# Kernel tuning notes

Hardware: AMD Instinct MI355X
Metric: run time of the kernel (lower is better)

## Reference

```python
import jax, jax.numpy as jnp
import numpy as np

S, B, D, H, V = 1024, 4, 1024, 4096, 32000
EPS = 1e-5

def _ln(x, g, b):
    m = jnp.mean(x, axis=-1, keepdims=True)
    v = jnp.var(x, axis=-1, keepdims=True)
    return (x - m) * jax.lax.rsqrt(v + EPS) * g + b

def setup_inputs() -> dict:
    key = jax.random.key(0)
    ks = jax.random.split(key, 12)
    def xav(k, shape):
        fan_in, fan_out = shape[1], shape[0]
        lim = np.sqrt(6.0 / (fan_in + fan_out))
        return jax.random.uniform(k, shape, jnp.float32, -lim, lim)
    return {
        "inputs": jax.random.randint(ks[0], (S, B), 0, V, dtype=jnp.int32),
        "emb_table": jax.random.normal(ks[1], (V, D), jnp.float32),
        "WQ": xav(ks[2], (D, D)),
        "WK": xav(ks[3], (D, D)),
        "WV": xav(ks[4], (D, D)),
        "Wo": xav(ks[5], (D, D)),
        "bo": jnp.zeros((D,), jnp.float32),
        "W1": xav(ks[6], (H, D)),
        "b1": jnp.zeros((H,), jnp.float32),
        "W2": xav(ks[7], (D, H)),
        "b2": jnp.zeros((D,), jnp.float32),
        "g1": jnp.ones((D,), jnp.float32),
        "be1": jnp.zeros((D,), jnp.float32),
        "g2": jnp.ones((D,), jnp.float32),
        "be2": jnp.zeros((D,), jnp.float32),
        "Wd": xav(ks[8], (V, D)),
        "bd": jnp.zeros((V,), jnp.float32),
    }

def reference(inputs, emb_table, WQ, WK, WV, Wo, bo, W1, b1, W2, b2, g1, be1, g2, be2, Wd, bd):
    # inputs: [S, B] int ids
    emb = emb_table[inputs]                       # [S, B, D]
    # F.linear(x, W) == x @ W.T
    Q = jnp.einsum('sbd,ed->bse', emb, WQ)        # [B, S, D]
    K = jnp.einsum('sbd,ed->bse', emb, WK)
    Vv = jnp.einsum('sbd,ed->bse', emb, WV)
    scores = jnp.einsum('bqd,bkd->bqk', Q, K) / jnp.sqrt(jnp.float32(D))
    attn = jax.nn.softmax(scores, axis=-1)        # [B, S, S]
    z = jnp.einsum('bqk,bkd->qbd', attn, Vv)      # back to [S, B, D]
    z = jnp.einsum('sbd,ed->sbe', z, Wo) + bo
    x = _ln(emb + z, g1, be1)
    ffn = jnp.einsum('sbh,dh->sbd', jax.nn.relu(jnp.einsum('sbd,hd->sbh', x, W1) + b1), W2) + b2
    out = _ln(x + ffn, g2, be2)
    logits = out.reshape(S * B, D) @ Wd.T + bd    # [S*B, V]
    return logits
```

## Files before the change

kernel.cpp:

```cpp
#include <hip/hip_runtime.h>

typedef float f32x4 __attribute__((ext_vector_type(4)));
typedef __bf16 bf16x8 __attribute__((ext_vector_type(8)));
typedef int i32x4 __attribute__((ext_vector_type(4)));
typedef unsigned short u16;
typedef unsigned short u16x4 __attribute__((ext_vector_type(4)));
typedef unsigned short u16x8 __attribute__((ext_vector_type(8)));
typedef unsigned int u32;

#define SEQ 1024
#define NBATCH 4
#define DM 1024
#define HD 4096
#define NV 32000
#define NT (SEQ * NBATCH)

__device__ __forceinline__ u16 f2bf(float f) {
  u32 u = __builtin_bit_cast(u32, f);
  return (u16)((u + 0x7FFFu + ((u >> 16) & 1u)) >> 16);
}

__global__ __launch_bounds__(256) void cast_bf16_kernel(const float* __restrict__ in,
                                                        u16* __restrict__ out, int n8) {
  int i = blockIdx.x * 256 + threadIdx.x;
  if (i >= n8) return;
  const f32x4* p = (const f32x4*)(in + (long)i * 8);
  f32x4 a = p[0], b = p[1];
  u16x8 o;
  o[0] = f2bf(a[0]); o[1] = f2bf(a[1]); o[2] = f2bf(a[2]); o[3] = f2bf(a[3]);
  o[4] = f2bf(b[0]); o[5] = f2bf(b[1]); o[6] = f2bf(b[2]); o[7] = f2bf(b[3]);
  *(u16x8*)(out + (long)i * 8) = o;
}

__global__ __launch_bounds__(256) void embed_kernel(const int* __restrict__ ids,
                                                    const float* __restrict__ tab,
                                                    float* __restrict__ ef,
                                                    u16* __restrict__ eh) {
  int t = blockIdx.x, tid = threadIdx.x;
  long id = ids[t];
  f32x4 v = *(const f32x4*)(tab + id * DM + tid * 4);
  *(f32x4*)(ef + (long)t * DM + tid * 4) = v;
  u16x4 h;
  h[0] = f2bf(v[0]); h[1] = f2bf(v[1]); h[2] = f2bf(v[2]); h[3] = f2bf(v[3]);
  *(u16x4*)(eh + (long)t * DM + tid * 4) = h;
}

__global__ __launch_bounds__(256) void softmax_kernel(const float* __restrict__ s,
                                                      u16* __restrict__ p) {
  int row = blockIdx.x, tid = threadIdx.x;
  const float* rp = s + (long)row * SEQ;
  f32x4 v = *(const f32x4*)(rp + tid * 4);
  float mx = fmaxf(fmaxf(v[0], v[1]), fmaxf(v[2], v[3]));
  for (int o = 32; o; o >>= 1) mx = fmaxf(mx, __shfl_xor(mx, o));
  __shared__ float red[4];
  if ((tid & 63) == 0) red[tid >> 6] = mx;
  __syncthreads();
  mx = fmaxf(fmaxf(red[0], red[1]), fmaxf(red[2], red[3]));
  const float sc = 0.03125f;
  f32x4 e;
  e[0] = expf((v[0] - mx) * sc); e[1] = expf((v[1] - mx) * sc);
  e[2] = expf((v[2] - mx) * sc); e[3] = expf((v[3] - mx) * sc);
  float sm = e[0] + e[1] + e[2] + e[3];
  for (int o = 32; o; o >>= 1) sm += __shfl_xor(sm, o);
  __syncthreads();
  if ((tid & 63) == 0) red[tid >> 6] = sm;
  __syncthreads();
  sm = red[0] + red[1] + red[2] + red[3];
  float inv = 1.0f / sm;
  u16x4 o4;
  o4[0] = f2bf(e[0] * inv); o4[1] = f2bf(e[1] * inv);
  o4[2] = f2bf(e[2] * inv); o4[3] = f2bf(e[3] * inv);
  *(u16x4*)(p + (long)row * SEQ + tid * 4) = o4;
}

__global__ __launch_bounds__(256) void ln_kernel(const float* __restrict__ in,
                                                 const float* __restrict__ g,
                                                 const float* __restrict__ be,
                                                 float* __restrict__ outf,
                                                 u16* __restrict__ outh) {
  int row = blockIdx.x, tid = threadIdx.x;
  f32x4 v = *(const f32x4*)(in + (long)row * DM + tid * 4);
  float s = v[0] + v[1] + v[2] + v[3];
  float q = v[0] * v[0] + v[1] * v[1] + v[2] * v[2] + v[3] * v[3];
  for (int o = 32; o; o >>= 1) { s += __shfl_xor(s, o); q += __shfl_xor(q, o); }
  __shared__ float rs_[4], rq_[4];
  if ((tid & 63) == 0) { rs_[tid >> 6] = s; rq_[tid >> 6] = q; }
  __syncthreads();
  s = rs_[0] + rs_[1] + rs_[2] + rs_[3];
  q = rq_[0] + rq_[1] + rq_[2] + rq_[3];
  float mean = s * (1.0f / DM);
  float var = q * (1.0f / DM) - mean * mean;
  float rstd = rsqrtf(var + 1e-5f);
  f32x4 gg = *(const f32x4*)(g + tid * 4);
  f32x4 bb = *(const f32x4*)(be + tid * 4);
  f32x4 y;
  y[0] = (v[0] - mean) * rstd * gg[0] + bb[0];
  y[1] = (v[1] - mean) * rstd * gg[1] + bb[1];
  y[2] = (v[2] - mean) * rstd * gg[2] + bb[2];
  y[3] = (v[3] - mean) * rstd * gg[3] + bb[3];
  if (outf) *(f32x4*)(outf + (long)row * DM + tid * 4) = y;
  if (outh) {
    u16x4 h;
    h[0] = f2bf(y[0]); h[1] = f2bf(y[1]); h[2] = f2bf(y[2]); h[3] = f2bf(y[3]);
    *(u16x4*)(outh + (long)row * DM + tid * 4) = h;
  }
}

__global__ __launch_bounds__(256) void ln_i8_kernel(const float* __restrict__ in,
                                                    const float* __restrict__ g,
                                                    const float* __restrict__ be,
                                                    char* __restrict__ q8,
                                                    float* __restrict__ scale) {
  int row = blockIdx.x, tid = threadIdx.x;
  f32x4 v = *(const f32x4*)(in + (long)row * DM + tid * 4);
  float s = v[0] + v[1] + v[2] + v[3];
  float q = v[0] * v[0] + v[1] * v[1] + v[2] * v[2] + v[3] * v[3];
  for (int o = 32; o; o >>= 1) { s += __shfl_xor(s, o); q += __shfl_xor(q, o); }
  __shared__ float rs_[4], rq_[4], rm_[4];
  if ((tid & 63) == 0) { rs_[tid >> 6] = s; rq_[tid >> 6] = q; }
  __syncthreads();
  s = rs_[0] + rs_[1] + rs_[2] + rs_[3];
  q = rq_[0] + rq_[1] + rq_[2] + rq_[3];
  float mean = s * (1.0f / DM);
  float var = q * (1.0f / DM) - mean * mean;
  float rstd = rsqrtf(var + 1e-5f);
  f32x4 gg = *(const f32x4*)(g + tid * 4);
  f32x4 bb = *(const f32x4*)(be + tid * 4);
  f32x4 y;
  y[0] = (v[0] - mean) * rstd * gg[0] + bb[0];
  y[1] = (v[1] - mean) * rstd * gg[1] + bb[1];
  y[2] = (v[2] - mean) * rstd * gg[2] + bb[2];
  y[3] = (v[3] - mean) * rstd * gg[3] + bb[3];
  float am = fmaxf(fmaxf(fabsf(y[0]), fabsf(y[1])), fmaxf(fabsf(y[2]), fabsf(y[3])));
  for (int o = 32; o; o >>= 1) am = fmaxf(am, __shfl_xor(am, o));
  __syncthreads();
  if ((tid & 63) == 0) rm_[tid >> 6] = am;
  __syncthreads();
  am = fmaxf(fmaxf(rm_[0], rm_[1]), fmaxf(rm_[2], rm_[3]));
  float inv = (am > 0.f) ? 127.f / am : 0.f;
  int q0 = (int)rintf(y[0] * inv), q1 = (int)rintf(y[1] * inv);
  int q2 = (int)rintf(y[2] * inv), q3 = (int)rintf(y[3] * inv);
  u32 pk = (q0 & 255) | ((q1 & 255) << 8) | ((q2 & 255) << 16) | ((u32)(q3 & 255) << 24);
  *(u32*)(q8 + (size_t)row * DM + tid * 4) = pk;
  if (tid == 0) scale[row] = am * (1.0f / 127.f);
}

__global__ __launch_bounds__(256) void rowq_i8_kernel(const float* __restrict__ in,
                                                      char* __restrict__ q8,
                                                      float* __restrict__ scale) {
  int row = blockIdx.x, tid = threadIdx.x;
  f32x4 v = *(const f32x4*)(in + (size_t)row * DM + tid * 4);
  float am = fmaxf(fmaxf(fabsf(v[0]), fabsf(v[1])), fmaxf(fabsf(v[2]), fabsf(v[3])));
  for (int o = 32; o; o >>= 1) am = fmaxf(am, __shfl_xor(am, o));
  __shared__ float rm_[4];
  if ((tid & 63) == 0) rm_[tid >> 6] = am;
  __syncthreads();
  am = fmaxf(fmaxf(rm_[0], rm_[1]), fmaxf(rm_[2], rm_[3]));
  float inv = (am > 0.f) ? 127.f / am : 0.f;
  int q0 = (int)rintf(v[0] * inv), q1 = (int)rintf(v[1] * inv);
  int q2 = (int)rintf(v[2] * inv), q3 = (int)rintf(v[3] * inv);
  u32 pk = (q0 & 255) | ((q1 & 255) << 8) | ((q2 & 255) << 16) | ((u32)(q3 & 255) << 24);
  *(u32*)(q8 + (size_t)row * DM + tid * 4) = pk;
  if (tid == 0) scale[row] = am * (1.0f / 127.f);
}

#define GLD(gp, lp)                                              \
  __builtin_amdgcn_global_load_lds(                              \
      (__attribute__((address_space(1))) void*)(gp),             \
      (__attribute__((address_space(3))) void*)(lp), 16, 0, 0)

#define BM 128
#define BN 128
#define BK 32

__global__ __launch_bounds__(256) void gemm_bt(
    const u16* __restrict__ A, const u16* __restrict__ B,
    float* __restrict__ Cf, u16* __restrict__ Ch,
    const float* __restrict__ bias, const float* __restrict__ resid,
    int K, int lda, int ldb, int ldc,
    long batA, long batB, long batC, int relu) {
  __shared__ u16 As[BM * BK];
  __shared__ u16 Bs[BN * BK];
  const int tid = threadIdx.x;
  const int bz = blockIdx.z;
  A += (long)bz * batA;
  B += (long)bz * batB;
  const long cbase = (long)bz * batC;
  const int row0 = blockIdx.y * BM;
  const int col0 = blockIdx.x * BN;
  const int l = tid & 63;
  const int w = tid >> 6;
  const int wr = (w >> 1) * 64, wc = (w & 1) * 64;

  f32x4 acc[4][4] = {};

  const u16* gA = A + (long)(row0 + (tid >> 2)) * lda + (tid & 3) * 8;
  const u16* gB = B + (long)(col0 + (tid >> 2)) * ldb + (tid & 3) * 8;
  const long a64 = (long)64 * lda, b64 = (long)64 * ldb;
  u16* lA = As + tid * 8;
  u16* lB = Bs + tid * 8;

  const int fr = l & 15;
  const int fk = (l >> 4) * 8;
  const u16* rA = As + (wr + fr) * BK + fk;
  const u16* rB = Bs + (wc + fr) * BK + fk;

  for (int k0 = 0; k0 < K; k0 += BK) {
    GLD(gA + k0, lA);
    GLD(gA + a64 + k0, lA + 2048);
    GLD(gB + k0, lB);
    GLD(gB + b64 + k0, lB + 2048);
    __syncthreads();
    bf16x8 af[4], bf[4];
#pragma unroll
    for (int m = 0; m < 4; ++m) af[m] = *(const bf16x8*)(rA + m * 16 * BK);
#pragma unroll
    for (int n = 0; n < 4; ++n) bf[n] = *(const bf16x8*)(rB + n * 16 * BK);
#pragma unroll
    for (int m = 0; m < 4; ++m)
#pragma unroll
      for (int n = 0; n < 4; ++n)
        acc[m][n] = __builtin_amdgcn_mfma_f32_16x16x32_bf16(af[m], bf[n], acc[m][n], 0, 0, 0);
    __syncthreads();
  }

  const int er = row0 + wr + ((l >> 4) << 2);
  const int ec = col0 + wc + (l & 15);
#pragma unroll
  for (int m = 0; m < 4; ++m) {
#pragma unroll
    for (int n = 0; n < 4; ++n) {
      f32x4 v = acc[m][n];
      const int c = ec + n * 16;
      float bv = bias ? bias[c] : 0.0f;
#pragma unroll
      for (int i = 0; i < 4; ++i) {
        const int r = er + m * 16 + i;
        float x = v[i] + bv;
        if (resid) x += resid[(long)r * ldc + c];
        if (relu) x = fmaxf(x, 0.0f);
        if (Cf) Cf[cbase + (long)r * ldc + c] = x;
        if (Ch) Ch[cbase + (long)r * ldc + c] = f2bf(x);
      }
    }
  }
}

__global__ __launch_bounds__(256) void gemm_i8(
    const char* __restrict__ A, const char* __restrict__ B,
    float* __restrict__ C, const float* __restrict__ sA, const float* __restrict__ sB,
    const float* __restrict__ bias, int K, int lda, int ldb, int ldc,
    int Mtiles, int Ntiles) {
  __shared__ __align__(16) char As[128 * 64];
  __shared__ __align__(16) char Bs[128 * 64];
  const int tid = threadIdx.x;

  const int nwg = gridDim.x;
  const int blk = blockIdx.x;
  const int cpx = nwg >> 3;
  const int wg = (blk & 7) * cpx + (blk >> 3);
  const int gsz = 4 * Ntiles;
  const int gid = wg / gsz;
  const int rem = wg - gid * gsz;
  const int row0 = (gid * 4 + (rem & 3)) * 128;
  const int col0 = (rem >> 2) * 128;

  const int l = tid & 63;
  const int w = tid >> 6;
  const int wr = (w >> 1) * 64, wc = (w & 1) * 64;

  const int srow = tid >> 2;
  const int sslot = (tid & 3) ^ ((srow >> 1) & 3);
  const char* gA = A + (size_t)(row0 + srow) * lda + sslot * 16;
  const char* gB = B + (size_t)(col0 + srow) * ldb + sslot * 16;
  const size_t a64 = (size_t)64 * lda, b64 = (size_t)64 * ldb;
  char* lA = As + tid * 16;
  char* lB = Bs + tid * 16;

  const int fr = l & 15;
  const int fsw = 16 * ((l >> 4) ^ ((fr >> 1) & 3));
  const char* rA = As + (wr + fr) * 64 + fsw;
  const char* rB = Bs + (wc + fr) * 64 + fsw;

  i32x4 acc[4][4] = {};

  for (int k0 = 0; k0 < K; k0 += 64) {
    GLD(gA + k0, lA);
    GLD(gA + a64 + k0, lA + 4096);
    GLD(gB + k0, lB);
    GLD(gB + b64 + k0, lB + 4096);
    __syncthreads();
    i32x4 af[4], bf[4];
#pragma unroll
    for (int m = 0; m < 4; ++m) af[m] = *(const i32x4*)(rA + m * 16 * 64);
#pragma unroll
    for (int n = 0; n < 4; ++n) bf[n] = *(const i32x4*)(rB + n * 16 * 64);
#pragma unroll
    for (int m = 0; m < 4; ++m)
#pragma unroll
      for (int n = 0; n < 4; ++n)
        acc[m][n] = __builtin_amdgcn_mfma_i32_16x16x64_i8(af[m], bf[n], acc[m][n], 0, 0, 0);
    __syncthreads();
  }

  const int er = row0 + wr + ((l >> 4) << 2);
  const int ec = col0 + wc + (l & 15);
#pragma unroll
  for (int m = 0; m < 4; ++m) {
#pragma unroll
    for (int n = 0; n < 4; ++n) {
      i32x4 v = acc[m][n];
      const int c = ec + n * 16;
      const float sb = sB[c];
      const float bv = bias ? bias[c] : 0.0f;
#pragma unroll
      for (int i = 0; i < 4; ++i) {
        const int r = er + m * 16 + i;
        C[(size_t)r * ldc + c] = (float)v[i] * (sA[r] * sb) + bv;
      }
    }
  }
}

#define DSB() __builtin_amdgcn_sched_barrier(0)
#define SBAR() __builtin_amdgcn_s_barrier()

template <int N0, int N1>
__device__ __forceinline__ void mfma16(f32x4 (&acc)[8][4], const bf16x8 (&af)[8],
                                       bf16x8 b0, bf16x8 b1) {
#pragma unroll
  for (int m = 0; m < 8; ++m) {
    acc[m][N0] = __builtin_amdgcn_mfma_f32_16x16x32_bf16(af[m], b0, acc[m][N0], 0, 0, 0);
    acc[m][N1] = __builtin_amdgcn_mfma_f32_16x16x32_bf16(af[m], b1, acc[m][N1], 0, 0, 0);
  }
}

__global__ __launch_bounds__(512, 2) void gemm256_bt(
    const u16* __restrict__ A, const u16* __restrict__ B,
    float* __restrict__ Cf, u16* __restrict__ Ch,
    const float* __restrict__ bias,
    int K, int lda, int ldb, int ldc, int Mtiles, int Ntiles, int relu) {
  __shared__ __align__(16) u16 As[2][2][128 * 64];
  __shared__ __align__(16) u16 Bs[2][2][256 * 32];
  const int tid = threadIdx.x;

  const int nwg = gridDim.x;
  const int blk = blockIdx.x;
  const int cpx = nwg >> 3;
  const int wg = (blk & 7) * cpx + (blk >> 3);
  const int gsz = 4 * Ntiles;
  const int gid = wg / gsz;
  const int rem = wg - gid * gsz;
  const int row0 = (gid * 4 + (rem & 3)) * 256;
  const int col0 = (rem >> 2) * 256;

  const int l = tid & 63;
  const int w = tid >> 6;
  const int wr = w >> 2;
  const int wc = w & 3;

  const int sArow = tid >> 3;
  const int sAcol = ((tid & 7) ^ ((sArow >> 1) & 7)) * 8;
  const int sBrow = tid >> 2;
  const int sBcol = ((tid & 3) ^ ((sBrow >> 2) & 3)) * 8;

  const u16* gA = A + (size_t)(row0 + sArow) * lda + sAcol;
  const u16* gB = B + (size_t)(col0 + sBrow) * ldb + sBcol;
  const size_t a64 = (size_t)64 * lda;
  const size_t b128 = (size_t)128 * ldb;

#define STAGE_A(buf, h, kt)                                          \
  do {                                                               \
    const u16* _g = gA + (size_t)(h) * 128 * lda + (size_t)(kt) * 64;\
    u16* _l = &As[buf][h][0] + tid * 8;                              \
    GLD(_g, _l);                                                     \
    GLD(_g + a64, _l + 4096);                                        \
  } while (0)
#define STAGE_B(buf, kk, kt)                                         \
  do {                                                               \
    const u16* _g = gB + (size_t)(kt) * 64 + (kk) * 32;              \
    u16* _l = &Bs[buf][kk][0] + tid * 8;                             \
    GLD(_g, _l);                                                     \
    GLD(_g + b128, _l + 4096);                                       \
  } while (0)

  const int fr = l & 15;
  const int g8 = (l >> 4) * 8;
  const int acp0 = g8 ^ (((fr >> 1) & 7) * 8);
  const int acp1 = (32 + g8) ^ (((fr >> 1) & 7) * 8);
  const int bcp = g8 ^ (((fr >> 2) & 3) * 8);

#define RA(buf, m, cp) (*(const bf16x8*)(&As[buf][wr][((m) * 16 + fr) * 64 + (cp)]))
#define RB(buf, n, kk) (*(const bf16x8*)(&Bs[buf][kk][(wc * 64 + (n) * 16 + fr) * 32 + bcp]))

  f32x4 acc[8][4] = {};
  bf16x8 a0[8], a1[8], bb0, bb1;

  const int nkt = K >> 6;
  const int nit = nkt >> 1;

  STAGE_A(0, 0, 0); STAGE_A(0, 1, 0);
  STAGE_B(0, 0, 0); STAGE_B(0, 1, 0);
  STAGE_B(1, 0, 1); STAGE_A(1, 0, 1);
  asm volatile("s_waitcnt vmcnt(4)"); DSB();
  SBAR();

  for (int i = 0; i < nit; ++i) {
    const int u = 2 * i + 1;
    const int v = (2 * i + 2 < nkt) ? 2 * i + 2 : nkt - 1;
    const int w2 = (2 * i + 3 < nkt) ? 2 * i + 3 : nkt - 1;

#pragma unroll
    for (int m = 0; m < 8; ++m) a0[m] = RA(0, m, acp0);
    bb0 = RB(0, 0, 0); bb1 = RB(0, 1, 0);
    STAGE_A(1, 1, u);
    SBAR();
    asm volatile("s_waitcnt lgkmcnt(0)"); DSB();
    __builtin_amdgcn_s_setprio(1);
    mfma16<0, 1>(acc, a0, bb0, bb1);
    __builtin_amdgcn_s_setprio(0);
    SBAR();
    bb0 = RB(0, 2, 0); bb1 = RB(0, 3, 0);
    STAGE_B(1, 1, u);
    asm volatile("s_waitcnt vmcnt(6)"); DSB();
    SBAR();
    asm volatile("s_waitcnt lgkmcnt(0)"); DSB();
    __builtin_amdgcn_s_setprio(1);
    mfma16<2, 3>(acc, a0, bb0, bb1);
    __builtin_amdgcn_s_setprio(0);
    SBAR();
#pragma unroll
    for (int m = 0; m < 8; ++m) a1[m] = RA(0, m, acp1);
    bb0 = RB(0, 0, 1); bb1 = RB(0, 1, 1);
    STAGE_B(0, 0, v);
    SBAR();
    asm volatile("s_waitcnt lgkmcnt(0)"); DSB();
    __builtin_amdgcn_s_setprio(1);
    mfma16<0, 1>(acc, a1, bb0, bb1);
    __builtin_amdgcn_s_setprio(0);
    SBAR();
    bb0 = RB(0, 2, 1); bb1 = RB(0, 3, 1);
    STAGE_A(0, 0, v);
    asm volatile("s_waitcnt vmcnt(6)"); DSB();
    SBAR();
    asm volatile("s_waitcnt lgkmcnt(0)"); DSB();
    __builtin_amdgcn_s_setprio(1);
    mfma16<2, 3>(acc, a1, bb0, bb1);
    __builtin_amdgcn_s_setprio(0);
    SBAR();
#pragma unroll
    for (int m = 0; m < 8; ++m) a0[m] = RA(1, m, acp0);
    bb0 = RB(1, 0, 0); bb1 = RB(1, 1, 0);
    STAGE_A(0, 1, v);
    SBAR();
    asm volatile("s_waitcnt lgkmcnt(0)"); DSB();
    __builtin_amdgcn_s_setprio(1);
    mfma16<0, 1>(acc, a0, bb0, bb1);
    __builtin_amdgcn_s_setprio(0);
    SBAR();
    bb0 = RB(1, 2, 0); bb1 = RB(1, 3, 0);
    STAGE_B(0, 1, v);
    asm volatile("s_waitcnt vmcnt(6)"); DSB();
    SBAR();
    asm volatile("s_waitcnt lgkmcnt(0)"); DSB();
    __builtin_amdgcn_s_setprio(1);
    mfma16<2, 3>(acc, a0, bb0, bb1);
    __builtin_amdgcn_s_setprio(0);
    SBAR();
#pragma unroll
    for (int m = 0; m < 8; ++m) a1[m] = RA(1, m, acp1);
    bb0 = RB(1, 0, 1); bb1 = RB(1, 1, 1);
    STAGE_B(1, 0, w2);
    SBAR();
    asm volatile("s_waitcnt lgkmcnt(0)"); DSB();
    __builtin_amdgcn_s_setprio(1);
    mfma16<0, 1>(acc, a1, bb0, bb1);
    __builtin_amdgcn_s_setprio(0);
    SBAR();
    bb0 = RB(1, 2, 1); bb1 = RB(1, 3, 1);
    STAGE_A(1, 0, w2);
    asm volatile("s_waitcnt vmcnt(6)"); DSB();
    SBAR();
    asm volatile("s_waitcnt lgkmcnt(0)"); DSB();
    __builtin_amdgcn_s_setprio(1);
    mfma16<2, 3>(acc, a1, bb0, bb1);
    __builtin_amdgcn_s_setprio(0);
    SBAR();
  }

  asm volatile("s_waitcnt vmcnt(0)"); DSB();

  const int er = row0 + wr * 128 + ((l >> 4) << 2);
  const int ec = col0 + wc * 64 + (l & 15);
#pragma unroll
  for (int m = 0; m < 8; ++m) {
#pragma unroll
    for (int n = 0; n < 4; ++n) {
      f32x4 vv = acc[m][n];
      const int c = ec + n * 16;
      float bv = bias ? bias[c] : 0.0f;
#pragma unroll
      for (int i = 0; i < 4; ++i) {
        const int r = er + m * 16 + i;
        float x = vv[i] + bv;
        if (relu) x = fmaxf(x, 0.0f);
        if (Cf) Cf[(size_t)r * ldc + c] = x;
        if (Ch) Ch[(size_t)r * ldc + c] = f2bf(x);
      }
    }
  }
#undef STAGE_A
#undef STAGE_B
#undef RA
#undef RB
}

extern "C" void kernel_launch(void* const* d_in, const int* in_sizes, int n_in,
                              void* d_out, int out_size, void* d_ws, size_t ws_size,
                              hipStream_t stream) {
  const int* ids = (const int*)d_in[0];
  const float* tab = (const float*)d_in[1];
  const float* WQ = (const float*)d_in[2];
  const float* WK = (const float*)d_in[3];
  const float* WV = (const float*)d_in[4];
  const float* Wo = (const float*)d_in[5];
  const float* bo = (const float*)d_in[6];
  const float* W1 = (const float*)d_in[7];
  const float* b1 = (const float*)d_in[8];
  const float* W2 = (const float*)d_in[9];
  const float* b2 = (const float*)d_in[10];
  const float* g1 = (const float*)d_in[11];
  const float* be1 = (const float*)d_in[12];
  const float* g2 = (const float*)d_in[13];
  const float* be2 = (const float*)d_in[14];
  const float* Wd = (const float*)d_in[15];
  const float* bd = (const float*)d_in[16];
  float* logits = (float*)d_out;

  if (ws_size < 280000000ull) return;

  char* p = (char*)d_ws;
  auto alloc = [&](size_t bytes) {
    char* r = p;
    p += (bytes + 255) & ~(size_t)255;
    return r;
  };
  float* embf = (float*)alloc((size_t)NT * DM * 4);
  u16* embh = (u16*)alloc((size_t)NT * DM * 2);
  u16* WQh = (u16*)alloc((size_t)DM * DM * 2);
  u16* WKh = (u16*)alloc((size_t)DM * DM * 2);
  u16* WVh = (u16*)alloc((size_t)DM * DM * 2);
  u16* Woh = (u16*)alloc((size_t)DM * DM * 2);
  u16* W1h = (u16*)alloc((size_t)HD * DM * 2);
  u16* W2h = (u16*)alloc((size_t)DM * HD * 2);
  char* Wdq = (char*)alloc((size_t)NV * DM);
  float* sWd = (float*)alloc((size_t)NV * 4);
  u16* Qh = (u16*)alloc((size_t)NT * DM * 2);
  u16* Kh = (u16*)alloc((size_t)NT * DM * 2);
  u16* VTh = (u16*)alloc((size_t)NBATCH * DM * SEQ * 2);
  float* scoresf = (float*)alloc((size_t)NBATCH * SEQ * SEQ * 4);
  u16* Ph = (u16*)alloc((size_t)NBATCH * SEQ * SEQ * 2);
  u16* zh = (u16*)alloc((size_t)NT * DM * 2);
  float* r1f = (float*)alloc((size_t)NT * DM * 4);
  float* xf = (float*)alloc((size_t)NT * DM * 4);
  u16* xh = (u16*)alloc((size_t)NT * DM * 2);
  u16* hh = (u16*)alloc((size_t)NT * HD * 2);
  float* r2f = (float*)alloc((size_t)NT * DM * 4);
  char* outq = (char*)alloc((size_t)NT * DM);
  float* sOut = (float*)alloc((size_t)NT * 4);

  cast_bf16_kernel<<<dim3(DM * DM / 8 / 256), 256, 0, stream>>>(WQ, WQh, DM * DM / 8);
  cast_bf16_kernel<<<dim3(DM * DM / 8 / 256), 256, 0, stream>>>(WK, WKh, DM * DM / 8);
  cast_bf16_kernel<<<dim3(DM * DM / 8 / 256), 256, 0, stream>>>(WV, WVh, DM * DM / 8);
  cast_bf16_kernel<<<dim3(DM * DM / 8 / 256), 256, 0, stream>>>(Wo, Woh, DM * DM / 8);
  cast_bf16_kernel<<<dim3(HD * DM / 8 / 256), 256, 0, stream>>>(W1, W1h, HD * DM / 8);
  cast_bf16_kernel<<<dim3(DM * HD / 8 / 256), 256, 0, stream>>>(W2, W2h, DM * HD / 8);
  rowq_i8_kernel<<<dim3(NV), 256, 0, stream>>>(Wd, Wdq, sWd);

  embed_kernel<<<NT, 256, 0, stream>>>(ids, tab, embf, embh);

  gemm_bt<<<dim3(DM / BN, NT / BM, 1), 256, 0, stream>>>(
      embh, WQh, nullptr, Qh, nullptr, nullptr, DM, DM, DM, DM, 0, 0, 0, 0);
  gemm_bt<<<dim3(DM / BN, NT / BM, 1), 256, 0, stream>>>(
      embh, WKh, nullptr, Kh, nullptr, nullptr, DM, DM, DM, DM, 0, 0, 0, 0);

  gemm_bt<<<dim3(SEQ / BN, DM / BM, NBATCH), 256, 0, stream>>>(
      WVh, embh, nullptr, VTh, nullptr, nullptr, DM, DM, NBATCH * DM, SEQ,
      0, DM, (long)DM * SEQ, 0);

  gemm_bt<<<dim3(SEQ / BN, SEQ / BM, NBATCH), 256, 0, stream>>>(
      Qh, Kh, scoresf, nullptr, nullptr, nullptr, DM, NBATCH * DM, NBATCH * DM, SEQ,
      DM, DM, (long)SEQ * SEQ, 0);

  softmax_kernel<<<NBATCH * SEQ, 256, 0, stream>>>(scoresf, Ph);

  gemm_bt<<<dim3(DM / BN, SEQ / BM, NBATCH), 256, 0, stream>>>(
      Ph, VTh, nullptr, zh, nullptr, nullptr, SEQ, SEQ, SEQ, NBATCH * DM,
      (long)SEQ * SEQ, (long)DM * SEQ, DM, 0);

  gemm_bt<<<dim3(DM / BN, NT / BM, 1), 256, 0, stream>>>(
      zh, Woh, r1f, nullptr, bo, embf, DM, DM, DM, DM, 0, 0, 0, 0);

  ln_kernel<<<NT, 256, 0, stream>>>(r1f, g1, be1, xf, xh);

  gemm256_bt<<<dim3((NT / 256) * (HD / 256)), 512, 0, stream>>>(
      xh, W1h, nullptr, hh, b1, DM, DM, DM, HD, NT / 256, HD / 256, 1);
  gemm_bt<<<dim3(DM / BN, NT / BM, 1), 256, 0, stream>>>(
      hh, W2h, r2f, nullptr, b2, xf, HD, HD, HD, DM, 0, 0, 0, 0);

  ln_i8_kernel<<<NT, 256, 0, stream>>>(r2f, g2, be2, outq, sOut);

  gemm_i8<<<dim3((NT / 128) * (NV / 128)), 256, 0, stream>>>(
      outq, Wdq, logits, sOut, sWd, bd, DM, DM, DM, NV, NT / 128, NV / 128);
}
```

Measured before the change: 794.5 us.

## Deepen int8 GEMM K-tile to 128 and fuse Q/K projections into one GEMM

The int8 logits GEMM now stages a 128-deep K slice per iteration, with a wider 8-slot XOR swizzle and two MFMA passes per tile. This halves the number of barrier pairs and loop iterations but doubles shared memory per block. Separately, the WQ and WK bf16 weights are concatenated so Q and K come from one GEMM launch writing an interleaved QK buffer. The scores GEMM reads that buffer with adjusted strides, which saves a launch and a second read of the embeddings.

```diff
diff --git a/kernel.cpp b/kernel.cpp
--- a/kernel.cpp
+++ b/kernel.cpp
@@ -251,8 +251,8 @@
     float* __restrict__ C, const float* __restrict__ sA, const float* __restrict__ sB,
     const float* __restrict__ bias, int K, int lda, int ldb, int ldc,
     int Mtiles, int Ntiles) {
-  __shared__ __align__(16) char As[128 * 64];
-  __shared__ __align__(16) char Bs[128 * 64];
+  __shared__ __align__(16) char As[128 * 128];
+  __shared__ __align__(16) char Bs[128 * 128];
   const int tid = threadIdx.x;
 
   const int nwg = gridDim.x;
@@ -269,32 +269,48 @@
   const int w = tid >> 6;
   const int wr = (w >> 1) * 64, wc = (w & 1) * 64;
 
-  const int srow = tid >> 2;
-  const int sslot = (tid & 3) ^ ((srow >> 1) & 3);
+  const int srow = tid >> 3;
+  const int sslot = (tid & 7) ^ ((tid >> 4) & 7);
   const char* gA = A + (size_t)(row0 + srow) * lda + sslot * 16;
   const char* gB = B + (size_t)(col0 + srow) * ldb + sslot * 16;
-  const size_t a64 = (size_t)64 * lda, b64 = (size_t)64 * ldb;
+  const size_t a32 = (size_t)32 * lda, b32 = (size_t)32 * ldb;
   char* lA = As + tid * 16;
   char* lB = Bs + tid * 16;
 
   const int fr = l & 15;
-  const int fsw = 16 * ((l >> 4) ^ ((fr >> 1) & 3));
-  const char* rA = As + (wr + fr) * 64 + fsw;
-  const char* rB = Bs + (wc + fr) * 64 + fsw;
+  const int g = l >> 4;
+  const int x = (fr >> 1) & 7;
+  const int sw0 = (g ^ x) * 16;
+  const int sw1 = ((4 + g) ^ x) * 16;
+  const char* rA = As + (wr + fr) * 128;
+  const char* rB = Bs + (wc + fr) * 128;
 
   i32x4 acc[4][4] = {};
 
-  for (int k0 = 0; k0 < K; k0 += 64) {
+  for (int k0 = 0; k0 < K; k0 += 128) {
     GLD(gA + k0, lA);
-    GLD(gA + a64 + k0, lA + 4096);
+    GLD(gA + k0 + a32, lA + 4096);
+    GLD(gA + k0 + 2 * a32, lA + 8192);
+    GLD(gA + k0 + 3 * a32, lA + 12288);
     GLD(gB + k0, lB);
-    GLD(gB + b64 + k0, lB + 4096);
+    GLD(gB + k0 + b32, lB + 4096);
+    GLD(gB + k0 + 2 * b32, lB + 8192);
+    GLD(gB + k0 + 3 * b32, lB + 12288);
     __syncthreads();
     i32x4 af[4], bf[4];
 #pragma unroll
-    for (int m = 0; m < 4; ++m) af[m] = *(const i32x4*)(rA + m * 16 * 64);
-#pragma unroll
-    for (int n = 0; n < 4; ++n) bf[n] = *(const i32x4*)(rB + n * 16 * 64);
+    for (int m = 0; m < 4; ++m) af[m] = *(const i32x4*)(rA + m * 2048 + sw0);
+#pragma unroll
+    for (int n = 0; n < 4; ++n) bf[n] = *(const i32x4*)(rB + n * 2048 + sw0);
+#pragma unroll
+    for (int m = 0; m < 4; ++m)
+#pragma unroll
+      for (int n = 0; n < 4; ++n)
+        acc[m][n] = __builtin_amdgcn_mfma_i32_16x16x64_i8(af[m], bf[n], acc[m][n], 0, 0, 0);
+#pragma unroll
+    for (int m = 0; m < 4; ++m) af[m] = *(const i32x4*)(rA + m * 2048 + sw1);
+#pragma unroll
+    for (int n = 0; n < 4; ++n) bf[n] = *(const i32x4*)(rB + n * 2048 + sw1);
 #pragma unroll
     for (int m = 0; m < 4; ++m)
 #pragma unroll
@@ -547,16 +563,14 @@
   };
   float* embf = (float*)alloc((size_t)NT * DM * 4);
   u16* embh = (u16*)alloc((size_t)NT * DM * 2);
-  u16* WQh = (u16*)alloc((size_t)DM * DM * 2);
-  u16* WKh = (u16*)alloc((size_t)DM * DM * 2);
+  u16* WQKh = (u16*)alloc((size_t)2 * DM * DM * 2);
   u16* WVh = (u16*)alloc((size_t)DM * DM * 2);
   u16* Woh = (u16*)alloc((size_t)DM * DM * 2);
   u16* W1h = (u16*)alloc((size_t)HD * DM * 2);
   u16* W2h = (u16*)alloc((size_t)DM * HD * 2);
   char* Wdq = (char*)alloc((size_t)NV * DM);
   float* sWd = (float*)alloc((size_t)NV * 4);
-  u16* Qh = (u16*)alloc((size_t)NT * DM * 2);
-  u16* Kh = (u16*)alloc((size_t)NT * DM * 2);
+  u16* QKh = (u16*)alloc((size_t)NT * 2 * DM * 2);
   u16* VTh = (u16*)alloc((size_t)NBATCH * DM * SEQ * 2);
   float* scoresf = (float*)alloc((size_t)NBATCH * SEQ * SEQ * 4);
   u16* Ph = (u16*)alloc((size_t)NBATCH * SEQ * SEQ * 2);
@@ -569,8 +583,8 @@
   char* outq = (char*)alloc((size_t)NT * DM);
   float* sOut = (float*)alloc((size_t)NT * 4);
 
-  cast_bf16_kernel<<<dim3(DM * DM / 8 / 256), 256, 0, stream>>>(WQ, WQh, DM * DM / 8);
-  cast_bf16_kernel<<<dim3(DM * DM / 8 / 256), 256, 0, stream>>>(WK, WKh, DM * DM / 8);
+  cast_bf16_kernel<<<dim3(DM * DM / 8 / 256), 256, 0, stream>>>(WQ, WQKh, DM * DM / 8);
+  cast_bf16_kernel<<<dim3(DM * DM / 8 / 256), 256, 0, stream>>>(WK, WQKh + (size_t)DM * DM, DM * DM / 8);
   cast_bf16_kernel<<<dim3(DM * DM / 8 / 256), 256, 0, stream>>>(WV, WVh, DM * DM / 8);
   cast_bf16_kernel<<<dim3(DM * DM / 8 / 256), 256, 0, stream>>>(Wo, Woh, DM * DM / 8);
   cast_bf16_kernel<<<dim3(HD * DM / 8 / 256), 256, 0, stream>>>(W1, W1h, HD * DM / 8);
@@ -579,18 +593,17 @@
 
   embed_kernel<<<NT, 256, 0, stream>>>(ids, tab, embf, embh);
 
-  gemm_bt<<<dim3(DM / BN, NT / BM, 1), 256, 0, stream>>>(
-      embh, WQh, nullptr, Qh, nullptr, nullptr, DM, DM, DM, DM, 0, 0, 0, 0);
-  gemm_bt<<<dim3(DM / BN, NT / BM, 1), 256, 0, stream>>>(
-      embh, WKh, nullptr, Kh, nullptr, nullptr, DM, DM, DM, DM, 0, 0, 0, 0);
+  gemm_bt<<<dim3(2 * DM / BN, NT / BM, 1), 256, 0, stream>>>(
+      embh, WQKh, nullptr, QKh, nullptr, nullptr, DM, DM, DM, 2 * DM, 0, 0, 0, 0);
 
   gemm_bt<<<dim3(SEQ / BN, DM / BM, NBATCH), 256, 0, stream>>>(
       WVh, embh, nullptr, VTh, nullptr, nullptr, DM, DM, NBATCH * DM, SEQ,
       0, DM, (long)DM * SEQ, 0);
 
   gemm_bt<<<dim3(SEQ / BN, SEQ / BM, NBATCH), 256, 0, stream>>>(
-      Qh, Kh, scoresf, nullptr, nullptr, nullptr, DM, NBATCH * DM, NBATCH * DM, SEQ,
-      DM, DM, (long)SEQ * SEQ, 0);
+      QKh, QKh + DM, scoresf, nullptr, nullptr, nullptr, DM,
+      NBATCH * 2 * DM, NBATCH * 2 * DM, SEQ,
+      2 * DM, 2 * DM, (long)SEQ * SEQ, 0);
 
   softmax_kernel<<<NBATCH * SEQ, 256, 0, stream>>>(scoresf, Ph);
 
```

New measurement: 763.3 us. 1.04x faster.
